# Kernel optimization log

Measured on AMD Instinct MI355X. Metric: run time of the kernel, lower is better.

The kernel has to match this reference:

```python
import jax, jax.numpy as jnp
import numpy as np

NUM_USERS = 200000
NUM_ITEMS = 100000
D = 128
NNZ = 2000000
L = 2  # opt['GNN']


def spmm(rows, cols, vals, x, n_out):
    # sparse [n_out, n_in] @ dense [n_in, d] via gather + segment_sum
    return jax.ops.segment_sum(vals[:, None] * x[cols], rows, num_segments=n_out)


def setup_inputs() -> dict:
    key = jax.random.key(0)
    ks = jax.random.split(key, 12)
    return {
        "ufea": jax.random.normal(ks[0], (NUM_USERS, D), jnp.float32),
        "vfea": jax.random.normal(ks[1], (NUM_ITEMS, D), jnp.float32),
        "uv_rows": jax.random.randint(ks[2], (NNZ,), 0, NUM_USERS, jnp.int32),
        "uv_cols": jax.random.randint(ks[3], (NNZ,), 0, NUM_ITEMS, jnp.int32),
        "uv_vals": jax.random.uniform(ks[4], (NNZ,), jnp.float32),
        "vu_rows": jax.random.randint(ks[5], (NNZ,), 0, NUM_ITEMS, jnp.int32),
        "vu_cols": jax.random.randint(ks[6], (NNZ,), 0, NUM_USERS, jnp.int32),
        "vu_vals": jax.random.uniform(ks[7], (NNZ,), jnp.float32),
        "user_W": jax.random.normal(ks[8], (L, 2 * D, D), jnp.float32) * 0.05,
        "user_b": jax.random.normal(ks[9], (L, D), jnp.float32) * 0.05,
        "item_W": jax.random.normal(ks[10], (L, 2 * D, D), jnp.float32) * 0.05,
        "item_b": jax.random.normal(ks[11], (L, D), jnp.float32) * 0.05,
    }


def reference(ufea, vfea, uv_rows, uv_cols, uv_vals,
              vu_rows, vu_cols, vu_vals,
              user_W, user_b, item_W, item_b):
    learn_user, learn_item = ufea, vfea
    for l in range(L):
        # dropout is identity at inference (training=False)
        # two-hop aggregation through the bipartite graph
        user_ho = spmm(vu_rows, vu_cols, vu_vals, learn_user, NUM_ITEMS)   # [I, D]
        item_ho = spmm(uv_rows, uv_cols, uv_vals, learn_item, NUM_USERS)   # [U, D]
        user_ho = spmm(uv_rows, uv_cols, uv_vals, user_ho, NUM_USERS)      # [U, D]
        item_ho = spmm(vu_rows, vu_cols, vu_vals, item_ho, NUM_ITEMS)      # [I, D]
        user_cat = jnp.concatenate([user_ho, learn_user], axis=1)          # [U, 2D]
        item_cat = jnp.concatenate([item_ho, learn_item], axis=1)          # [I, 2D]
        learn_user = jax.nn.relu(user_cat @ user_W[l] + user_b[l])
        learn_item = jax.nn.relu(item_cat @ item_W[l] + item_b[l])
    return learn_user, learn_item
```

## Files before the change

kernel.cpp:

```cpp
#include <hip/hip_runtime.h>

#define DIM 128
#define N_USERS 200000
#define N_ITEMS 100000
#define CAP_U 40
#define CAP_I 56

typedef __attribute__((ext_vector_type(8))) _Float16 half8;
typedef __attribute__((ext_vector_type(4))) _Float16 half4v;
typedef __attribute__((ext_vector_type(4))) float f32x4;

__global__ __launch_bounds__(256) void scatter_ell_dual_kernel(
    const int* __restrict__ rowsA, const int* __restrict__ colsA,
    const float* __restrict__ valsA, int* __restrict__ degA,
    int2* __restrict__ ellA, int capA, int nA, int rloA, int rhiA,
    const int* __restrict__ rowsB, const int* __restrict__ colsB,
    const float* __restrict__ valsB, int* __restrict__ degB,
    int2* __restrict__ ellB, int capB, int nB, int rloB, int rhiB)
{
    int stride = gridDim.x * blockDim.x;
    int t0 = blockIdx.x * blockDim.x + threadIdx.x;

    int nA4 = nA >> 2;
    for (int q = t0; q < nA4; q += stride) {
        int4   r = reinterpret_cast<const int4*>(rowsA)[q];
        int4   c = reinterpret_cast<const int4*>(colsA)[q];
        float4 v = reinterpret_cast<const float4*>(valsA)[q];
        if (r.x >= rloA && r.x < rhiA) { int s = atomicAdd(&degA[r.x], 1); if (s < capA) ellA[(size_t)r.x * capA + s] = make_int2(c.x, __float_as_int(v.x)); }
        if (r.y >= rloA && r.y < rhiA) { int s = atomicAdd(&degA[r.y], 1); if (s < capA) ellA[(size_t)r.y * capA + s] = make_int2(c.y, __float_as_int(v.y)); }
        if (r.z >= rloA && r.z < rhiA) { int s = atomicAdd(&degA[r.z], 1); if (s < capA) ellA[(size_t)r.z * capA + s] = make_int2(c.z, __float_as_int(v.z)); }
        if (r.w >= rloA && r.w < rhiA) { int s = atomicAdd(&degA[r.w], 1); if (s < capA) ellA[(size_t)r.w * capA + s] = make_int2(c.w, __float_as_int(v.w)); }
    }
    for (int t = (nA4 << 2) + t0; t < nA; t += stride) {
        int r = rowsA[t];
        if (r >= rloA && r < rhiA) {
            int s = atomicAdd(&degA[r], 1);
            if (s < capA) ellA[(size_t)r * capA + s] = make_int2(colsA[t], __float_as_int(valsA[t]));
        }
    }

    int nB4 = nB >> 2;
    for (int q = t0; q < nB4; q += stride) {
        int4   r = reinterpret_cast<const int4*>(rowsB)[q];
        int4   c = reinterpret_cast<const int4*>(colsB)[q];
        float4 v = reinterpret_cast<const float4*>(valsB)[q];
        if (r.x >= rloB && r.x < rhiB) { int s = atomicAdd(&degB[r.x], 1); if (s < capB) ellB[(size_t)r.x * capB + s] = make_int2(c.x, __float_as_int(v.x)); }
        if (r.y >= rloB && r.y < rhiB) { int s = atomicAdd(&degB[r.y], 1); if (s < capB) ellB[(size_t)r.y * capB + s] = make_int2(c.y, __float_as_int(v.y)); }
        if (r.z >= rloB && r.z < rhiB) { int s = atomicAdd(&degB[r.z], 1); if (s < capB) ellB[(size_t)r.z * capB + s] = make_int2(c.z, __float_as_int(v.z)); }
        if (r.w >= rloB && r.w < rhiB) { int s = atomicAdd(&degB[r.w], 1); if (s < capB) ellB[(size_t)r.w * capB + s] = make_int2(c.w, __float_as_int(v.w)); }
    }
    for (int t = (nB4 << 2) + t0; t < nB; t += stride) {
        int r = rowsB[t];
        if (r >= rloB && r < rhiB) {
            int s = atomicAdd(&degB[r], 1);
            if (s < capB) ellB[(size_t)r * capB + s] = make_int2(colsB[t], __float_as_int(valsB[t]));
        }
    }
}

__global__ __launch_bounds__(256) void conv_dual_kernel(
    const float* __restrict__ srcA, _Float16* __restrict__ dstA, int n8A,
    const float* __restrict__ srcB, _Float16* __restrict__ dstB, int n8B)
{
    int t = blockIdx.x * blockDim.x + threadIdx.x;
    const float* src;
    _Float16* dst;
    if (t < n8A) { src = srcA; dst = dstA; }
    else {
        t -= n8A;
        if (t >= n8B) return;
        src = srcB; dst = dstB;
    }
    const float4* s = reinterpret_cast<const float4*>(src) + (size_t)t * 2;
    float4 a = s[0], b = s[1];
    half8 h;
    h[0] = (_Float16)a.x; h[1] = (_Float16)a.y;
    h[2] = (_Float16)a.z; h[3] = (_Float16)a.w;
    h[4] = (_Float16)b.x; h[5] = (_Float16)b.y;
    h[6] = (_Float16)b.z; h[7] = (_Float16)b.w;
    reinterpret_cast<half8*>(dst)[t] = h;
}

__global__ __launch_bounds__(256) void transposeW_dual_kernel(
    const float* __restrict__ Wu, _Float16* __restrict__ Wtu,
    const float* __restrict__ Wi, _Float16* __restrict__ Wti)
{
    int t = blockIdx.x * blockDim.x + threadIdx.x;
    const float* W;
    _Float16* Wt;
    if (t < 65536) { W = Wu; Wt = Wtu; }
    else           { W = Wi; Wt = Wti; t -= 65536; }
    int l = t >> 15;
    int r = t & 32767;
    int k = r >> 7;
    int n = r & 127;
    Wt[(size_t)l * 32768 + n * 256 + k] = (_Float16)W[t];
}

__global__ __launch_bounds__(256) void spmm_dual_kernel(
    const int* __restrict__ degA, const int2* __restrict__ ellA, int capA,
    const _Float16* __restrict__ xA, _Float16* __restrict__ outA, int nA,
    const int* __restrict__ degB, const int2* __restrict__ ellB, int capB,
    const _Float16* __restrict__ xB, _Float16* __restrict__ outB, int nB)
{
    int t    = blockIdx.x * blockDim.x + threadIdx.x;
    int grp  = t >> 4;
    int lane = t & 15;

    const int2*     edg;
    const _Float16* x;
    _Float16*       out;
    int row, cnt;
    if (grp < nA) {
        row = grp;
        cnt = min(degA[row], capA);
        edg = ellA + (size_t)row * capA;
        x = xA; out = outA;
    } else {
        row = grp - nA;
        if (row >= nB) return;
        cnt = min(degB[row], capB);
        edg = ellB + (size_t)row * capB;
        x = xB; out = outB;
    }

    float acc[8] = {0.f, 0.f, 0.f, 0.f, 0.f, 0.f, 0.f, 0.f};
    int k = 0;
    for (; k + 7 < cnt; k += 8) {
        int2 e[8];
        half8 xv[8];
#pragma unroll
        for (int u = 0; u < 8; ++u) e[u] = edg[k + u];
#pragma unroll
        for (int u = 0; u < 8; ++u)
            xv[u] = *reinterpret_cast<const half8*>(
                x + (size_t)e[u].x * DIM + lane * 8);
#pragma unroll
        for (int u = 0; u < 8; ++u) {
            float v = __int_as_float(e[u].y);
#pragma unroll
            for (int i = 0; i < 8; ++i) acc[i] += v * (float)xv[u][i];
        }
    }
    if (k + 3 < cnt) {
        int2 e[4];
        half8 xv[4];
#pragma unroll
        for (int u = 0; u < 4; ++u) e[u] = edg[k + u];
#pragma unroll
        for (int u = 0; u < 4; ++u)
            xv[u] = *reinterpret_cast<const half8*>(
                x + (size_t)e[u].x * DIM + lane * 8);
#pragma unroll
        for (int u = 0; u < 4; ++u) {
            float v = __int_as_float(e[u].y);
#pragma unroll
            for (int i = 0; i < 8; ++i) acc[i] += v * (float)xv[u][i];
        }
        k += 4;
    }
    for (; k < cnt; ++k) {
        int2 e0 = edg[k];
        half8 x0 = *reinterpret_cast<const half8*>(x + (size_t)e0.x * DIM + lane * 8);
        float v0 = __int_as_float(e0.y);
#pragma unroll
        for (int i = 0; i < 8; ++i) acc[i] += v0 * (float)x0[i];
    }
    half8 o;
#pragma unroll
    for (int i = 0; i < 8; ++i) o[i] = (_Float16)acc[i];
    *reinterpret_cast<half8*>(out + (size_t)row * DIM + lane * 8) = o;
}

template<int OUT_F32>
__global__ __launch_bounds__(256) void gemm_dual_kernel(
    const _Float16* __restrict__ HOu, const _Float16* __restrict__ CURu,
    const _Float16* __restrict__ Wtu, const float* __restrict__ bu,
    float* __restrict__ outFu, _Float16* __restrict__ outHu, int Mu, int ublocks,
    const _Float16* __restrict__ HOi, const _Float16* __restrict__ CURi,
    const _Float16* __restrict__ Wti, const float* __restrict__ bi,
    float* __restrict__ outFi, _Float16* __restrict__ outHi, int Mi)
{
    const int TILES = 8;
    int bid = blockIdx.x;
    const _Float16 *HO, *CUR, *Wt;
    const float* bias;
    float* outF;
    _Float16* outH;
    int M;
    if (bid < ublocks) {
        HO = HOu; CUR = CURu; Wt = Wtu; bias = bu; outF = outFu; outH = outHu; M = Mu;
    } else {
        bid -= ublocks;
        HO = HOi; CUR = CURi; Wt = Wti; bias = bi; outF = outFi; outH = outHi; M = Mi;
    }

    int tid  = threadIdx.x;
    int wave = tid >> 6;
    int l    = tid & 63;
    int m    = l & 15;
    int kg   = l >> 4;

    half8 wfrag[2][8];
    float4 bv[2];
#pragma unroll
    for (int jj = 0; jj < 2; ++jj) {
        int j = wave * 2 + jj;
#pragma unroll
        for (int kk = 0; kk < 8; ++kk)
            wfrag[jj][kk] = *reinterpret_cast<const half8*>(
                Wt + (size_t)(j * 16 + m) * 256 + kk * 32 + kg * 8);
        bv[jj] = *reinterpret_cast<const float4*>(bias + j * 16 + kg * 4);
    }

    int base = bid * (TILES * 16);
#pragma unroll 2
    for (int t = 0; t < TILES; ++t) {
        int row = base + t * 16 + m;
        int rr  = min(row, M - 1);
        half8 afrag[8];
#pragma unroll
        for (int kk = 0; kk < 8; ++kk) {
            const _Float16* src = (kk < 4) ? HO : CUR;
            int k0 = (kk & 3) * 32 + kg * 8;
            afrag[kk] = *reinterpret_cast<const half8*>(src + (size_t)rr * DIM + k0);
        }
#pragma unroll
        for (int jj = 0; jj < 2; ++jj) {
            f32x4 acc = {0.f, 0.f, 0.f, 0.f};
#pragma unroll
            for (int kk = 0; kk < 8; ++kk)
                acc = __builtin_amdgcn_mfma_f32_16x16x32_f16(
                    wfrag[jj][kk], afrag[kk], acc, 0, 0, 0);
            int n0 = (wave * 2 + jj) * 16 + kg * 4;
            float o0 = fmaxf(acc[0] + bv[jj].x, 0.f);
            float o1 = fmaxf(acc[1] + bv[jj].y, 0.f);
            float o2 = fmaxf(acc[2] + bv[jj].z, 0.f);
            float o3 = fmaxf(acc[3] + bv[jj].w, 0.f);
            if (row < M) {
                if (OUT_F32) {
                    float4 st = make_float4(o0, o1, o2, o3);
                    *reinterpret_cast<float4*>(outF + (size_t)row * DIM + n0) = st;
                } else {
                    half4v st;
                    st[0] = (_Float16)o0; st[1] = (_Float16)o1;
                    st[2] = (_Float16)o2; st[3] = (_Float16)o3;
                    *reinterpret_cast<half4v*>(outH + (size_t)row * DIM + n0) = st;
                }
            }
        }
    }
}

extern "C" void kernel_launch(void* const* d_in, const int* in_sizes, int n_in,
                              void* d_out, int out_size, void* d_ws, size_t ws_size,
                              hipStream_t stream) {
    const float* ufea    = (const float*)d_in[0];
    const float* vfea    = (const float*)d_in[1];
    const int*   uv_rows = (const int*)d_in[2];
    const int*   uv_cols = (const int*)d_in[3];
    const float* uv_vals = (const float*)d_in[4];
    const int*   vu_rows = (const int*)d_in[5];
    const int*   vu_cols = (const int*)d_in[6];
    const float* vu_vals = (const float*)d_in[7];
    const float* user_W  = (const float*)d_in[8];
    const float* user_b  = (const float*)d_in[9];
    const float* item_W  = (const float*)d_in[10];
    const float* item_b  = (const float*)d_in[11];

    const int nnz = in_sizes[2];

    float* out_user = (float*)d_out;
    float* out_item = out_user + (size_t)N_USERS * DIM;

    const size_t UD = (size_t)N_USERS * DIM;
    const size_t ID = (size_t)N_ITEMS * DIM;

    char* p = (char*)d_ws;
    auto alloc = [&](size_t bytes) {
        char* q = p;
        p += (bytes + 255) & ~(size_t)255;
        return q;
    };
    _Float16* Uf = (_Float16*)alloc(UD * 2);
    _Float16* Vf = (_Float16*)alloc(ID * 2);
    _Float16* Ua = (_Float16*)alloc(UD * 2);
    _Float16* Ub = (_Float16*)alloc(UD * 2);
    _Float16* Va = (_Float16*)alloc(ID * 2);
    _Float16* Vb = (_Float16*)alloc(ID * 2);
    _Float16* Vc = (_Float16*)alloc(ID * 2);
    _Float16* Wt_user = (_Float16*)alloc((size_t)2 * 128 * 256 * 2);
    _Float16* Wt_item = (_Float16*)alloc((size_t)2 * 128 * 256 * 2);
    int* deg_all = (int*)alloc((size_t)(N_USERS + N_ITEMS) * 4);
    int* uv_deg  = deg_all;
    int* vu_deg  = deg_all + N_USERS;
    int2* uv_ell = (int2*)alloc((size_t)N_USERS * CAP_U * 8);
    int2* vu_ell = (int2*)alloc((size_t)N_ITEMS * CAP_I * 8);

    _Float16* Uc = (_Float16*)out_item;

    {
        int n8A = (int)(UD / 8), n8B = (int)(ID / 8);
        conv_dual_kernel<<<(n8A + n8B + 255) / 256, 256, 0, stream>>>(
            ufea, Uf, n8A, vfea, Vf, n8B);
        transposeW_dual_kernel<<<512, 256, 0, stream>>>(user_W, Wt_user,
                                                        item_W, Wt_item);
    }

    {
        const int GS_BLOCKS = 2048;
        hipMemsetAsync(deg_all, 0, (size_t)(N_USERS + N_ITEMS) * 4, stream);
        const int NPASS = 4;
        int wU = (N_USERS + NPASS - 1) / NPASS;
        int wI = (N_ITEMS + NPASS - 1) / NPASS;
        for (int pass = 0; pass < NPASS; ++pass) {
            scatter_ell_dual_kernel<<<GS_BLOCKS, 256, 0, stream>>>(
                uv_rows, uv_cols, uv_vals, uv_deg, uv_ell, CAP_U, nnz,
                pass * wU, min((pass + 1) * wU, N_USERS),
                vu_rows, vu_cols, vu_vals, vu_deg, vu_ell, CAP_I, nnz,
                pass * wI, min((pass + 1) * wI, N_ITEMS));
        }
    }

    auto spmm_pair = [&](const _Float16* xu, _Float16* outI,
                         const _Float16* xv, _Float16* outU) {
        size_t groups = (size_t)N_ITEMS + N_USERS;
        int blocks = (int)((groups * 16 + 255) / 256);
        spmm_dual_kernel<<<blocks, 256, 0, stream>>>(
            vu_deg, vu_ell, CAP_I, xu, outI, N_ITEMS,
            uv_deg, uv_ell, CAP_U, xv, outU, N_USERS);
    };

    const int UB = (N_USERS + 127) / 128;
    const int IB = (N_ITEMS + 127) / 128;

    spmm_pair(Uf, Va, Vf, Ua);
    spmm_pair(Ua, Vb, Va, Ub);
    gemm_dual_kernel<0><<<UB + IB, 256, 0, stream>>>(
        Ub, Uf, Wt_user, user_b, (float*)nullptr, Ua, N_USERS, UB,
        Vb, Vf, Wt_item, item_b, (float*)nullptr, Va, N_ITEMS);

    spmm_pair(Ua, Vb, Va, Ub);
    spmm_pair(Ub, Vc, Vb, Uc);
    gemm_dual_kernel<1><<<UB, 256, 0, stream>>>(
        Uc, Ua, Wt_user + 32768, user_b + DIM, out_user, (_Float16*)nullptr, N_USERS, UB,
        Uc, Ua, Wt_user + 32768, user_b + DIM, out_user, (_Float16*)nullptr, N_USERS);
    gemm_dual_kernel<1><<<IB, 256, 0, stream>>>(
        Vc, Va, Wt_item + 32768, item_b + DIM, out_item, (_Float16*)nullptr, N_ITEMS, IB,
        Vc, Va, Wt_item + 32768, item_b + DIM, out_item, (_Float16*)nullptr, N_ITEMS);
}
```

Before: 1.096 ms.

## Sort SpMM rows by degree via counting sort to balance wavefront work

Adds a three-kernel counting sort that buckets rows by degree into permutation arrays. SpMM thread groups then process rows in permuted order, so each wavefront sees rows with similar edge counts and less lane divergence. The 8-way unrolled edge loop is replaced by a 4-way loop. In exchange there are three extra launches, an extra indirection per row, and scattered output writes.

```diff
diff --git a/kernel.cpp b/kernel.cpp
--- a/kernel.cpp
+++ b/kernel.cpp
@@ -5,6 +5,7 @@
 #define N_ITEMS 100000
 #define CAP_U 40
 #define CAP_I 56
+#define NBIN 64
 
 typedef __attribute__((ext_vector_type(8))) _Float16 half8;
 typedef __attribute__((ext_vector_type(4))) _Float16 half4v;
@@ -54,6 +55,76 @@
         if (r >= rloB && r < rhiB) {
             int s = atomicAdd(&degB[r], 1);
             if (s < capB) ellB[(size_t)r * capB + s] = make_int2(colsB[t], __float_as_int(valsB[t]));
+        }
+    }
+}
+
+
+__global__ __launch_bounds__(256) void sort1_dual_kernel(
+    const int* __restrict__ degU, int* __restrict__ cntU, int nU, int nbU,
+    const int* __restrict__ degI, int* __restrict__ cntI, int nI, int nbI)
+{
+    __shared__ int hist[NBIN];
+    const int* deg; int* cnt; int n, nb, blk;
+    if ((int)blockIdx.x < nbU) { deg = degU; cnt = cntU; n = nU; nb = nbU; blk = blockIdx.x; }
+    else { deg = degI; cnt = cntI; n = nI; nb = nbI; blk = blockIdx.x - nbU; }
+
+    if (threadIdx.x < NBIN) hist[threadIdx.x] = 0;
+    __syncthreads();
+    int base = blk * 1024 + threadIdx.x * 4;
+#pragma unroll
+    for (int i = 0; i < 4; ++i) {
+        int r = base + i;
+        if (r < n) atomicAdd(&hist[min(deg[r], NBIN - 1)], 1);
+    }
+    __syncthreads();
+    if (threadIdx.x < NBIN) cnt[threadIdx.x * nb + blk] = hist[threadIdx.x];
+}
+
+__global__ __launch_bounds__(256) void sort2_dual_kernel(
+    int* __restrict__ cntU, int totU, int* __restrict__ cntI, int totI)
+{
+    __shared__ int part[256];
+    int* a = (blockIdx.x == 0) ? cntU : cntI;
+    int n  = (blockIdx.x == 0) ? totU : totI;
+    int tid = threadIdx.x;
+    int chunk = (n + 255) / 256;
+    int lo = tid * chunk, hi = min(lo + chunk, n);
+    int s = 0;
+    for (int i = lo; i < hi; ++i) s += a[i];
+    part[tid] = s;
+    __syncthreads();
+    for (int d = 1; d < 256; d <<= 1) {
+        int t = 0;
+        if (tid >= d) t = part[tid - d];
+        __syncthreads();
+        part[tid] += t;
+        __syncthreads();
+    }
+    int run = (tid > 0) ? part[tid - 1] : 0;
+    for (int i = lo; i < hi; ++i) { int v = a[i]; a[i] = run; run += v; }
+}
+
+__global__ __launch_bounds__(256) void sort3_dual_kernel(
+    const int* __restrict__ degU, const int* __restrict__ cntU,
+    int* __restrict__ permU, int nU, int nbU,
+    const int* __restrict__ degI, const int* __restrict__ cntI,
+    int* __restrict__ permI, int nI, int nbI)
+{
+    __shared__ int cur[NBIN];
+    const int* deg; const int* cnt; int* perm; int n, nb, blk;
+    if ((int)blockIdx.x < nbU) { deg = degU; cnt = cntU; perm = permU; n = nU; nb = nbU; blk = blockIdx.x; }
+    else { deg = degI; cnt = cntI; perm = permI; n = nI; nb = nbI; blk = blockIdx.x - nbU; }
+
+    if (threadIdx.x < NBIN) cur[threadIdx.x] = cnt[threadIdx.x * nb + blk];
+    __syncthreads();
+    int base = blk * 1024 + threadIdx.x * 4;
+#pragma unroll
+    for (int i = 0; i < 4; ++i) {
+        int r = base + i;
+        if (r < n) {
+            int p = atomicAdd(&cur[min(deg[r], NBIN - 1)], 1);
+            perm[p] = r;
         }
     }
 }
@@ -99,8 +170,10 @@
 
 __global__ __launch_bounds__(256) void spmm_dual_kernel(
     const int* __restrict__ degA, const int2* __restrict__ ellA, int capA,
+    const int* __restrict__ permA,
     const _Float16* __restrict__ xA, _Float16* __restrict__ outA, int nA,
     const int* __restrict__ degB, const int2* __restrict__ ellB, int capB,
+    const int* __restrict__ permB,
     const _Float16* __restrict__ xB, _Float16* __restrict__ outB, int nB)
 {
     int t    = blockIdx.x * blockDim.x + threadIdx.x;
@@ -112,13 +185,14 @@
     _Float16*       out;
     int row, cnt;
     if (grp < nA) {
-        row = grp;
+        row = permA[grp];
         cnt = min(degA[row], capA);
         edg = ellA + (size_t)row * capA;
         x = xA; out = outA;
     } else {
-        row = grp - nA;
-        if (row >= nB) return;
+        int g = grp - nA;
+        if (g >= nB) return;
+        row = permB[g];
         cnt = min(degB[row], capB);
         edg = ellB + (size_t)row * capB;
         x = xB; out = outB;
@@ -126,23 +200,7 @@
 
     float acc[8] = {0.f, 0.f, 0.f, 0.f, 0.f, 0.f, 0.f, 0.f};
     int k = 0;
-    for (; k + 7 < cnt; k += 8) {
-        int2 e[8];
-        half8 xv[8];
-#pragma unroll
-        for (int u = 0; u < 8; ++u) e[u] = edg[k + u];
-#pragma unroll
-        for (int u = 0; u < 8; ++u)
-            xv[u] = *reinterpret_cast<const half8*>(
-                x + (size_t)e[u].x * DIM + lane * 8);
-#pragma unroll
-        for (int u = 0; u < 8; ++u) {
-            float v = __int_as_float(e[u].y);
-#pragma unroll
-            for (int i = 0; i < 8; ++i) acc[i] += v * (float)xv[u][i];
-        }
-    }
-    if (k + 3 < cnt) {
+    for (; k + 3 < cnt; k += 4) {
         int2 e[4];
         half8 xv[4];
 #pragma unroll
@@ -157,7 +215,6 @@
 #pragma unroll
             for (int i = 0; i < 8; ++i) acc[i] += v * (float)xv[u][i];
         }
-        k += 4;
     }
     for (; k < cnt; ++k) {
         int2 e0 = edg[k];
@@ -296,6 +353,12 @@
     int* vu_deg  = deg_all + N_USERS;
     int2* uv_ell = (int2*)alloc((size_t)N_USERS * CAP_U * 8);
     int2* vu_ell = (int2*)alloc((size_t)N_ITEMS * CAP_I * 8);
+    int* perm_u  = (int*)alloc((size_t)N_USERS * 4);
+    int* perm_i  = (int*)alloc((size_t)N_ITEMS * 4);
+    const int nbU = (N_USERS + 1023) / 1024;
+    const int nbI = (N_ITEMS + 1023) / 1024;
+    int* cntU = (int*)alloc((size_t)NBIN * nbU * 4);
+    int* cntI = (int*)alloc((size_t)NBIN * nbI * 4);
 
     _Float16* Uc = (_Float16*)out_item;
 
@@ -322,13 +385,20 @@
         }
     }
 
+    sort1_dual_kernel<<<nbU + nbI, 256, 0, stream>>>(
+        uv_deg, cntU, N_USERS, nbU, vu_deg, cntI, N_ITEMS, nbI);
+    sort2_dual_kernel<<<2, 256, 0, stream>>>(cntU, NBIN * nbU, cntI, NBIN * nbI);
+    sort3_dual_kernel<<<nbU + nbI, 256, 0, stream>>>(
+        uv_deg, cntU, perm_u, N_USERS, nbU,
+        vu_deg, cntI, perm_i, N_ITEMS, nbI);
+
     auto spmm_pair = [&](const _Float16* xu, _Float16* outI,
                          const _Float16* xv, _Float16* outU) {
         size_t groups = (size_t)N_ITEMS + N_USERS;
         int blocks = (int)((groups * 16 + 255) / 256);
         spmm_dual_kernel<<<blocks, 256, 0, stream>>>(
-            vu_deg, vu_ell, CAP_I, xu, outI, N_ITEMS,
-            uv_deg, uv_ell, CAP_U, xv, outU, N_USERS);
+            vu_deg, vu_ell, CAP_I, perm_i, xu, outI, N_ITEMS,
+            uv_deg, uv_ell, CAP_U, perm_u, xv, outU, N_USERS);
     };
 
     const int UB = (N_USERS + 127) / 128;
```

Result: slower. 1.129 ms (+3.0%).

## Compact ELL adjacency to CSR and fuse setup kernels with scatter passes

Applied to the files above, without the earlier changes.

Adds a prefix scan over clamped degrees and a pack kernel that copies the padded ELL rows into a compact CSR array, so the SpMM kernels read contiguous edge lists bounded by row offsets instead of strided padded rows. The fp16 conversion and weight transpose are folded into the first two scatter launches as extra blocks, which cuts launch count and lets that work overlap with the scatter. The final layer's two GEMMs are merged into one dual launch by reusing the Uf buffer for the last SpMM output. In exchange it adds scan and pack kernels and a full copy of the edge data, and the CSR buffers are placed in the output memory ahead of the GEMM writes.

```diff
diff --git a/kernel.cpp b/kernel.cpp
--- a/kernel.cpp
+++ b/kernel.cpp
@@ -5,22 +5,23 @@
 #define N_ITEMS 100000
 #define CAP_U 40
 #define CAP_I 56
+#define SCAT_BLOCKS 2048
+#define CONV_BLOCKS 512
+#define TRANS_BLOCKS 128
 
 typedef __attribute__((ext_vector_type(8))) _Float16 half8;
 typedef __attribute__((ext_vector_type(4))) _Float16 half4v;
 typedef __attribute__((ext_vector_type(4))) float f32x4;
 
-__global__ __launch_bounds__(256) void scatter_ell_dual_kernel(
+__device__ __forceinline__ void scatter_body(
     const int* __restrict__ rowsA, const int* __restrict__ colsA,
     const float* __restrict__ valsA, int* __restrict__ degA,
     int2* __restrict__ ellA, int capA, int nA, int rloA, int rhiA,
     const int* __restrict__ rowsB, const int* __restrict__ colsB,
     const float* __restrict__ valsB, int* __restrict__ degB,
-    int2* __restrict__ ellB, int capB, int nB, int rloB, int rhiB)
-{
-    int stride = gridDim.x * blockDim.x;
-    int t0 = blockIdx.x * blockDim.x + threadIdx.x;
-
+    int2* __restrict__ ellB, int capB, int nB, int rloB, int rhiB,
+    int t0, int stride)
+{
     int nA4 = nA >> 2;
     for (int q = t0; q < nA4; q += stride) {
         int4   r = reinterpret_cast<const int4*>(rowsA)[q];
@@ -38,7 +39,6 @@
             if (s < capA) ellA[(size_t)r * capA + s] = make_int2(colsA[t], __float_as_int(valsA[t]));
         }
     }
-
     int nB4 = nB >> 2;
     for (int q = t0; q < nB4; q += stride) {
         int4   r = reinterpret_cast<const int4*>(rowsB)[q];
@@ -58,91 +58,199 @@
     }
 }
 
-__global__ __launch_bounds__(256) void conv_dual_kernel(
-    const float* __restrict__ srcA, _Float16* __restrict__ dstA, int n8A,
-    const float* __restrict__ srcB, _Float16* __restrict__ dstB, int n8B)
-{
-    int t = blockIdx.x * blockDim.x + threadIdx.x;
-    const float* src;
-    _Float16* dst;
-    if (t < n8A) { src = srcA; dst = dstA; }
-    else {
-        t -= n8A;
-        if (t >= n8B) return;
-        src = srcB; dst = dstB;
-    }
-    const float4* s = reinterpret_cast<const float4*>(src) + (size_t)t * 2;
-    float4 a = s[0], b = s[1];
-    half8 h;
-    h[0] = (_Float16)a.x; h[1] = (_Float16)a.y;
-    h[2] = (_Float16)a.z; h[3] = (_Float16)a.w;
-    h[4] = (_Float16)b.x; h[5] = (_Float16)b.y;
-    h[6] = (_Float16)b.z; h[7] = (_Float16)b.w;
-    reinterpret_cast<half8*>(dst)[t] = h;
-}
-
-__global__ __launch_bounds__(256) void transposeW_dual_kernel(
+__global__ __launch_bounds__(256) void scatter_conv_kernel(
+    const int* rowsA, const int* colsA, const float* valsA, int* degA,
+    int2* ellA, int capA, int nA, int rloA, int rhiA,
+    const int* rowsB, const int* colsB, const float* valsB, int* degB,
+    int2* ellB, int capB, int nB, int rloB, int rhiB,
+    const float* __restrict__ srcU, _Float16* __restrict__ dstU, int n8U,
+    const float* __restrict__ srcV, _Float16* __restrict__ dstV, int n8V)
+{
+    if ((int)blockIdx.x < SCAT_BLOCKS) {
+        scatter_body(rowsA, colsA, valsA, degA, ellA, capA, nA, rloA, rhiA,
+                     rowsB, colsB, valsB, degB, ellB, capB, nB, rloB, rhiB,
+                     blockIdx.x * 256 + threadIdx.x, SCAT_BLOCKS * 256);
+        return;
+    }
+    int t0 = (blockIdx.x - SCAT_BLOCKS) * 256 + threadIdx.x;
+    int stride = CONV_BLOCKS * 256;
+    int total = n8U + n8V;
+    for (int t = t0; t < total; t += stride) {
+        const float* src; _Float16* dst; int i;
+        if (t < n8U) { src = srcU; dst = dstU; i = t; }
+        else         { src = srcV; dst = dstV; i = t - n8U; }
+        const float4* s = reinterpret_cast<const float4*>(src) + (size_t)i * 2;
+        float4 a = s[0], b = s[1];
+        half8 h;
+        h[0] = (_Float16)a.x; h[1] = (_Float16)a.y;
+        h[2] = (_Float16)a.z; h[3] = (_Float16)a.w;
+        h[4] = (_Float16)b.x; h[5] = (_Float16)b.y;
+        h[6] = (_Float16)b.z; h[7] = (_Float16)b.w;
+        reinterpret_cast<half8*>(dst)[i] = h;
+    }
+}
+
+__global__ __launch_bounds__(256) void scatter_trans_kernel(
+    const int* rowsA, const int* colsA, const float* valsA, int* degA,
+    int2* ellA, int capA, int nA, int rloA, int rhiA,
+    const int* rowsB, const int* colsB, const float* valsB, int* degB,
+    int2* ellB, int capB, int nB, int rloB, int rhiB,
     const float* __restrict__ Wu, _Float16* __restrict__ Wtu,
     const float* __restrict__ Wi, _Float16* __restrict__ Wti)
 {
+    if ((int)blockIdx.x < SCAT_BLOCKS) {
+        scatter_body(rowsA, colsA, valsA, degA, ellA, capA, nA, rloA, rhiA,
+                     rowsB, colsB, valsB, degB, ellB, capB, nB, rloB, rhiB,
+                     blockIdx.x * 256 + threadIdx.x, SCAT_BLOCKS * 256);
+        return;
+    }
+    int t0 = (blockIdx.x - SCAT_BLOCKS) * 256 + threadIdx.x;
+    int stride = TRANS_BLOCKS * 256;
+    for (int t = t0; t < 131072; t += stride) {
+        const float* W; _Float16* Wt; int i;
+        if (t < 65536) { W = Wu; Wt = Wtu; i = t; }
+        else           { W = Wi; Wt = Wti; i = t - 65536; }
+        int l = i >> 15;
+        int r = i & 32767;
+        int k = r >> 7;
+        int n = r & 127;
+        Wt[(size_t)l * 32768 + n * 256 + k] = (_Float16)W[i];
+    }
+}
+
+__global__ __launch_bounds__(256) void scatter_plain_kernel(
+    const int* rowsA, const int* colsA, const float* valsA, int* degA,
+    int2* ellA, int capA, int nA, int rloA, int rhiA,
+    const int* rowsB, const int* colsB, const float* valsB, int* degB,
+    int2* ellB, int capB, int nB, int rloB, int rhiB)
+{
+    scatter_body(rowsA, colsA, valsA, degA, ellA, capA, nA, rloA, rhiA,
+                 rowsB, colsB, valsB, degB, ellB, capB, nB, rloB, rhiB,
+                 blockIdx.x * 256 + threadIdx.x, gridDim.x * 256);
+}
+
+__global__ __launch_bounds__(256) void scan1_dual_kernel(
+    const int* __restrict__ degU, int* __restrict__ offU, int* __restrict__ bsU,
+    int nU, int nbU, int capU,
+    const int* __restrict__ degI, int* __restrict__ offI, int* __restrict__ bsI,
+    int nI, int nbI, int capI)
+{
+    __shared__ int lds[256];
+    const int* deg; int* out; int* bs; int n, blk, cap;
+    if ((int)blockIdx.x < nbU) { deg = degU; out = offU; bs = bsU; n = nU; blk = blockIdx.x; cap = capU; }
+    else { deg = degI; out = offI; bs = bsI; n = nI; blk = blockIdx.x - nbU; cap = capI; }
+
+    int tid  = threadIdx.x;
+    int base = blk * 1024 + tid * 4;
+    int v0 = (base + 0 < n) ? min(deg[base + 0], cap) : 0;
+    int v1 = (base + 1 < n) ? min(deg[base + 1], cap) : 0;
+    int v2 = (base + 2 < n) ? min(deg[base + 2], cap) : 0;
+    int v3 = (base + 3 < n) ? min(deg[base + 3], cap) : 0;
+    int s1 = v0 + v1, s2 = s1 + v2, s3 = s2 + v3;
+    lds[tid] = s3;
+    __syncthreads();
+    for (int d = 1; d < 256; d <<= 1) {
+        int t = 0;
+        if (tid >= d) t = lds[tid - d];
+        __syncthreads();
+        lds[tid] += t;
+        __syncthreads();
+    }
+    int excl = (tid > 0) ? lds[tid - 1] : 0;
+    if (base + 0 < n) out[base + 1] = excl + v0;
+    if (base + 1 < n) out[base + 2] = excl + s1;
+    if (base + 2 < n) out[base + 3] = excl + s2;
+    if (base + 3 < n) out[base + 4] = excl + s3;
+    if (tid == 255) bs[blk] = lds[255];
+    if (blk == 0 && tid == 0) out[0] = 0;
+}
+
+__global__ __launch_bounds__(256) void scan2_dual_kernel(
+    int* __restrict__ bsU, int nbU, int* __restrict__ bsI, int nbI)
+{
+    __shared__ int part[256];
+    int* a = (blockIdx.x == 0) ? bsU : bsI;
+    int n  = (blockIdx.x == 0) ? nbU : nbI;
+    int tid = threadIdx.x;
+    int v = (tid < n) ? a[tid] : 0;
+    part[tid] = v;
+    __syncthreads();
+    for (int d = 1; d < 256; d <<= 1) {
+        int t = 0;
+        if (tid >= d) t = part[tid - d];
+        __syncthreads();
+        part[tid] += t;
+        __syncthreads();
+    }
+    if (tid < n) a[tid] = (tid > 0) ? part[tid - 1] : 0;
+}
+
+__global__ __launch_bounds__(256) void scan3_dual_kernel(
+    int* __restrict__ offU, const int* __restrict__ bsU, int nU, int nbU,
+    int* __restrict__ offI, const int* __restrict__ bsI, int nI, int nbI)
+{
+    int* out; const int* bs; int n, blk;
+    if ((int)blockIdx.x < nbU) { out = offU; bs = bsU; n = nU; blk = blockIdx.x; }
+    else { out = offI; bs = bsI; n = nI; blk = blockIdx.x - nbU; }
+    int add  = bs[blk];
+    if (add == 0) return;
+    int base = blk * 1024 + threadIdx.x * 4;
+    if (base + 0 < n) out[base + 1] += add;
+    if (base + 1 < n) out[base + 2] += add;
+    if (base + 2 < n) out[base + 3] += add;
+    if (base + 3 < n) out[base + 4] += add;
+}
+
+__global__ __launch_bounds__(256) void pack_dual_kernel(
+    const int* __restrict__ degU, const int* __restrict__ offU,
+    const int2* __restrict__ ellU, int2* __restrict__ csrU, int nU,
+    const int* __restrict__ degI, const int* __restrict__ offI,
+    const int2* __restrict__ ellI, int2* __restrict__ csrI, int nI)
+{
     int t = blockIdx.x * blockDim.x + threadIdx.x;
-    const float* W;
-    _Float16* Wt;
-    if (t < 65536) { W = Wu; Wt = Wtu; }
-    else           { W = Wi; Wt = Wti; t -= 65536; }
-    int l = t >> 15;
-    int r = t & 32767;
-    int k = r >> 7;
-    int n = r & 127;
-    Wt[(size_t)l * 32768 + n * 256 + k] = (_Float16)W[t];
+    int g = t >> 2, lane = t & 3;
+    const int2* src; int2* dst; int d;
+    if (g < nU) {
+        d = min(degU[g], CAP_U);
+        src = ellU + (size_t)g * CAP_U;
+        dst = csrU + offU[g];
+    } else {
+        g -= nU;
+        if (g >= nI) return;
+        d = min(degI[g], CAP_I);
+        src = ellI + (size_t)g * CAP_I;
+        dst = csrI + offI[g];
+    }
+    for (int s = lane; s < d; s += 4) dst[s] = src[s];
 }
 
 __global__ __launch_bounds__(256) void spmm_dual_kernel(
-    const int* __restrict__ degA, const int2* __restrict__ ellA, int capA,
+    const int* __restrict__ offA, const int2* __restrict__ edgA,
     const _Float16* __restrict__ xA, _Float16* __restrict__ outA, int nA,
-    const int* __restrict__ degB, const int2* __restrict__ ellB, int capB,
+    const int* __restrict__ offB, const int2* __restrict__ edgB,
     const _Float16* __restrict__ xB, _Float16* __restrict__ outB, int nB)
 {
     int t    = blockIdx.x * blockDim.x + threadIdx.x;
     int grp  = t >> 4;
     int lane = t & 15;
 
+    const int*      off;
     const int2*     edg;
     const _Float16* x;
     _Float16*       out;
-    int row, cnt;
+    int row;
     if (grp < nA) {
-        row = grp;
-        cnt = min(degA[row], capA);
-        edg = ellA + (size_t)row * capA;
-        x = xA; out = outA;
+        off = offA; edg = edgA; x = xA; out = outA; row = grp;
     } else {
         row = grp - nA;
         if (row >= nB) return;
-        cnt = min(degB[row], capB);
-        edg = ellB + (size_t)row * capB;
-        x = xB; out = outB;
-    }
-
+        off = offB; edg = edgB; x = xB; out = outB;
+    }
+
+    int beg = off[row], end = off[row + 1];
     float acc[8] = {0.f, 0.f, 0.f, 0.f, 0.f, 0.f, 0.f, 0.f};
-    int k = 0;
-    for (; k + 7 < cnt; k += 8) {
-        int2 e[8];
-        half8 xv[8];
-#pragma unroll
-        for (int u = 0; u < 8; ++u) e[u] = edg[k + u];
-#pragma unroll
-        for (int u = 0; u < 8; ++u)
-            xv[u] = *reinterpret_cast<const half8*>(
-                x + (size_t)e[u].x * DIM + lane * 8);
-#pragma unroll
-        for (int u = 0; u < 8; ++u) {
-            float v = __int_as_float(e[u].y);
-#pragma unroll
-            for (int i = 0; i < 8; ++i) acc[i] += v * (float)xv[u][i];
-        }
-    }
-    if (k + 3 < cnt) {
+    int k = beg;
+    for (; k + 3 < end; k += 4) {
         int2 e[4];
         half8 xv[4];
 #pragma unroll
@@ -157,9 +265,8 @@
 #pragma unroll
             for (int i = 0; i < 8; ++i) acc[i] += v * (float)xv[u][i];
         }
-        k += 4;
-    }
-    for (; k < cnt; ++k) {
+    }
+    for (; k < end; ++k) {
         int2 e0 = edg[k];
         half8 x0 = *reinterpret_cast<const half8*>(x + (size_t)e0.x * DIM + lane * 8);
         float v0 = __int_as_float(e0.y);
@@ -296,30 +403,51 @@
     int* vu_deg  = deg_all + N_USERS;
     int2* uv_ell = (int2*)alloc((size_t)N_USERS * CAP_U * 8);
     int2* vu_ell = (int2*)alloc((size_t)N_ITEMS * CAP_I * 8);
-
-    _Float16* Uc = (_Float16*)out_item;
+    int* uv_off  = (int*)alloc((size_t)(N_USERS + 1) * 4);
+    int* vu_off  = (int*)alloc((size_t)(N_ITEMS + 1) * 4);
+    int* bsU     = (int*)alloc(256 * 4);
+    int* bsI     = (int*)alloc(256 * 4);
+
+    int2* uv_csr = (int2*)d_out;
+    int2* vu_csr = uv_csr + nnz;
+
+    const int nbU = (N_USERS + 1023) / 1024;
+    const int nbI = (N_ITEMS + 1023) / 1024;
 
     {
-        int n8A = (int)(UD / 8), n8B = (int)(ID / 8);
-        conv_dual_kernel<<<(n8A + n8B + 255) / 256, 256, 0, stream>>>(
-            ufea, Uf, n8A, vfea, Vf, n8B);
-        transposeW_dual_kernel<<<512, 256, 0, stream>>>(user_W, Wt_user,
-                                                        item_W, Wt_item);
-    }
-
-    {
-        const int GS_BLOCKS = 2048;
         hipMemsetAsync(deg_all, 0, (size_t)(N_USERS + N_ITEMS) * 4, stream);
         const int NPASS = 4;
         int wU = (N_USERS + NPASS - 1) / NPASS;
         int wI = (N_ITEMS + NPASS - 1) / NPASS;
-        for (int pass = 0; pass < NPASS; ++pass) {
-            scatter_ell_dual_kernel<<<GS_BLOCKS, 256, 0, stream>>>(
+
+        scatter_conv_kernel<<<SCAT_BLOCKS + CONV_BLOCKS, 256, 0, stream>>>(
+            uv_rows, uv_cols, uv_vals, uv_deg, uv_ell, CAP_U, nnz, 0, wU,
+            vu_rows, vu_cols, vu_vals, vu_deg, vu_ell, CAP_I, nnz, 0, wI,
+            ufea, Uf, (int)(UD / 8), vfea, Vf, (int)(ID / 8));
+        scatter_trans_kernel<<<SCAT_BLOCKS + TRANS_BLOCKS, 256, 0, stream>>>(
+            uv_rows, uv_cols, uv_vals, uv_deg, uv_ell, CAP_U, nnz, wU, 2 * wU,
+            vu_rows, vu_cols, vu_vals, vu_deg, vu_ell, CAP_I, nnz, wI, 2 * wI,
+            user_W, Wt_user, item_W, Wt_item);
+        for (int pass = 2; pass < NPASS; ++pass) {
+            scatter_plain_kernel<<<SCAT_BLOCKS, 256, 0, stream>>>(
                 uv_rows, uv_cols, uv_vals, uv_deg, uv_ell, CAP_U, nnz,
                 pass * wU, min((pass + 1) * wU, N_USERS),
                 vu_rows, vu_cols, vu_vals, vu_deg, vu_ell, CAP_I, nnz,
                 pass * wI, min((pass + 1) * wI, N_ITEMS));
         }
+    }
+
+    scan1_dual_kernel<<<nbU + nbI, 256, 0, stream>>>(
+        uv_deg, uv_off, bsU, N_USERS, nbU, CAP_U,
+        vu_deg, vu_off, bsI, N_ITEMS, nbI, CAP_I);
+    scan2_dual_kernel<<<2, 256, 0, stream>>>(bsU, nbU, bsI, nbI);
+    scan3_dual_kernel<<<nbU + nbI, 256, 0, stream>>>(
+        uv_off, bsU, N_USERS, nbU, vu_off, bsI, N_ITEMS, nbI);
+    {
+        int threads = (N_USERS + N_ITEMS) * 4;
+        pack_dual_kernel<<<(threads + 255) / 256, 256, 0, stream>>>(
+            uv_deg, uv_off, uv_ell, uv_csr, N_USERS,
+            vu_deg, vu_off, vu_ell, vu_csr, N_ITEMS);
     }
 
     auto spmm_pair = [&](const _Float16* xu, _Float16* outI,
@@ -327,8 +455,8 @@
         size_t groups = (size_t)N_ITEMS + N_USERS;
         int blocks = (int)((groups * 16 + 255) / 256);
         spmm_dual_kernel<<<blocks, 256, 0, stream>>>(
-            vu_deg, vu_ell, CAP_I, xu, outI, N_ITEMS,
-            uv_deg, uv_ell, CAP_U, xv, outU, N_USERS);
+            vu_off, vu_csr, xu, outI, N_ITEMS,
+            uv_off, uv_csr, xv, outU, N_USERS);
     };
 
     const int UB = (N_USERS + 127) / 128;
@@ -341,11 +469,8 @@
         Vb, Vf, Wt_item, item_b, (float*)nullptr, Va, N_ITEMS);
 
     spmm_pair(Ua, Vb, Va, Ub);
-    spmm_pair(Ub, Vc, Vb, Uc);
-    gemm_dual_kernel<1><<<UB, 256, 0, stream>>>(
-        Uc, Ua, Wt_user + 32768, user_b + DIM, out_user, (_Float16*)nullptr, N_USERS, UB,
-        Uc, Ua, Wt_user + 32768, user_b + DIM, out_user, (_Float16*)nullptr, N_USERS);
-    gemm_dual_kernel<1><<<IB, 256, 0, stream>>>(
-        Vc, Va, Wt_item + 32768, item_b + DIM, out_item, (_Float16*)nullptr, N_ITEMS, IB,
+    spmm_pair(Ub, Vc, Vb, Uf);
+    gemm_dual_kernel<1><<<UB + IB, 256, 0, stream>>>(
+        Uf, Ua, Wt_user + 32768, user_b + DIM, out_user, (_Float16*)nullptr, N_USERS, UB,
         Vc, Va, Wt_item + 32768, item_b + DIM, out_item, (_Float16*)nullptr, N_ITEMS);
 }
```

New measurement: 1.089 ms. No clear change (-0.6%).
